# Performance work log

Measured on AMD Instinct MI355X. Metric: run time of the kernel, lower is better.

The kernel has to match this reference:

```python
import jax, jax.numpy as jnp
import numpy as np

E = 1024; H = 16; D = E // H; MAX_LEN = 512; B = 4; N = 1024
EPS = 1e-5
NEG_INF = float('-inf')


def layernorm(x, g, b):
    mu = jnp.mean(x, axis=-1, keepdims=True)
    var = jnp.mean((x - mu) ** 2, axis=-1, keepdims=True)
    return (x - mu) * jax.lax.rsqrt(var + EPS) * g + b


def rel_bias(seq_len, rel_pos):
    # rel_pos: (H, MAX_LEN). bias[h,i,j] = rel_pos[h, i-j] if 0<=i-j<MAX_LEN else -inf
    pos = jnp.arange(seq_len)
    rel = pos[:, None] - pos[None, :]                     # (N, N)
    valid = (rel >= 0) & (rel < rel_pos.shape[-1])
    idx = jnp.clip(rel, 0, rel_pos.shape[-1] - 1)
    gathered = rel_pos[:, idx]                            # (H, N, N)
    return jnp.where(valid[None], gathered, NEG_INF)


def setup_inputs() -> dict:
    key = jax.random.key(0)
    ks = jax.random.split(key, 12)
    s = 0.02
    return {
        'x': jax.random.normal(ks[0], (B, N, E), jnp.float32),
        'rel_pos': jax.random.normal(ks[1], (H, MAX_LEN), jnp.float32),
        'in_proj_w': jax.random.normal(ks[2], (3 * E, E), jnp.float32) * s,
        'in_proj_b': jnp.zeros((3 * E,), jnp.float32),
        'out_w': jax.random.normal(ks[3], (E, E), jnp.float32) * s,
        'out_b': jnp.zeros((E,), jnp.float32),
        'w1': jax.random.normal(ks[4], (4 * E, E), jnp.float32) * s,
        'b1': jnp.zeros((4 * E,), jnp.float32),
        'w2': jax.random.normal(ks[5], (E, 4 * E), jnp.float32) * s,
        'b2': jnp.zeros((E,), jnp.float32),
        'ln1_g': jnp.ones((E,), jnp.float32),
        'ln1_b': jnp.zeros((E,), jnp.float32),
        'ln2_g': jnp.ones((E,), jnp.float32),
        'ln2_b': jnp.zeros((E,), jnp.float32),
    }


def reference(x, rel_pos, in_proj_w, in_proj_b, out_w, out_b,
              w1, b1, w2, b2, ln1_g, ln1_b, ln2_g, ln2_b):
    b, n, e = x.shape
    xn = layernorm(x, ln1_g, ln1_b)
    qkv = xn @ in_proj_w.T + in_proj_b                    # (B, N, 3E)
    q, k, v = jnp.split(qkv, 3, axis=-1)
    # (B, N, E) -> (B, H, N, D)
    def heads(t):
        return t.reshape(b, n, H, D).transpose(0, 2, 1, 3)
    q, k, v = heads(q), heads(k), heads(v)
    bias = rel_bias(n, rel_pos)                           # (H, N, N)
    scores = jnp.einsum('bhnd,bhmd->bhnm', q, k) / np.sqrt(D) + bias[None]
    attn = jax.nn.softmax(scores, axis=-1)
    o = jnp.einsum('bhnm,bhmd->bhnd', attn, v)            # (B, H, N, D)
    o = o.transpose(0, 2, 1, 3).reshape(b, n, e)
    x = x + o @ out_w.T + out_b
    xm = layernorm(x, ln2_g, ln2_b)
    h = jax.nn.relu(xm @ w1.T + b1)
    return x + h @ w2.T + b2
```

## Files before the change

### kernel.cpp

```cpp
#include <hip/hip_runtime.h>
#include <math.h>

#define BB 4
#define NN 1024
#define EE 1024
#define HH 16
#define DD 64
#define MAXLEN 512
#define EPS 1e-5f

typedef __attribute__((ext_vector_type(8))) __bf16 bf16x8;
typedef __attribute__((ext_vector_type(4))) float floatx4;
typedef __attribute__((ext_vector_type(8))) unsigned short ushort8;

#define SWAIT(s) asm volatile("s_waitcnt " s ::: "memory")
#define SCHEDBAR() __builtin_amdgcn_sched_barrier(0)

__device__ __forceinline__ unsigned short f2bf(float f) {
    unsigned u = __float_as_uint(f);
    u += 0x7fffu + ((u >> 16) & 1u);
    return (unsigned short)(u >> 16);
}

template <int MAXR>
__device__ __forceinline__ void vm_wait_rt(int rem) {
    if (rem >= MAXR) {
        if constexpr (MAXR <= 0)      SWAIT("vmcnt(0)");
        else if constexpr (MAXR == 1) SWAIT("vmcnt(4)");
        else if constexpr (MAXR == 2) SWAIT("vmcnt(8)");
        else                          SWAIT("vmcnt(12)");
        return;
    }
    if (rem <= 0) { SWAIT("vmcnt(0)"); return; }
    if (rem == 1) { SWAIT("vmcnt(4)"); return; }
    if constexpr (MAXR >= 3) { if (rem == 2) { SWAIT("vmcnt(8)");  return; } }
}

__global__ __launch_bounds__(256) void f2bf_all_kernel(
    const float* __restrict__ s0, const float* __restrict__ s1,
    const float* __restrict__ s2, const float* __restrict__ s3,
    unsigned short* __restrict__ d0, unsigned short* __restrict__ d1,
    unsigned short* __restrict__ d2, unsigned short* __restrict__ d3) {
    const int C0 = 3 * EE * EE / 4;
    const int C1 = C0 + EE * EE / 4;
    const int C2 = C1 + EE * EE;
    int i = blockIdx.x * 256 + threadIdx.x;
    const float* in; unsigned short* out; int j;
    if (i < C0)      { in = s0; out = d0; j = i; }
    else if (i < C1) { in = s1; out = d1; j = i - C0; }
    else if (i < C2) { in = s2; out = d2; j = i - C1; }
    else             { in = s3; out = d3; j = i - C2; }
    float4 v = ((const float4*)in)[j];
    ushort4 o;
    o.x = f2bf(v.x); o.y = f2bf(v.y); o.z = f2bf(v.z); o.w = f2bf(v.w);
    ((ushort4*)out)[j] = o;
}

__global__ __launch_bounds__(256) void ln_kernel(const float* __restrict__ x,
                                                 const float* __restrict__ g,
                                                 const float* __restrict__ b,
                                                 unsigned short* __restrict__ out) {
    const int row = blockIdx.x;
    const int tid = threadIdx.x;
    const float4 v = ((const float4*)(x + (size_t)row * EE))[tid];
    float s  = v.x + v.y + v.z + v.w;
    float s2 = v.x * v.x + v.y * v.y + v.z * v.z + v.w * v.w;
    for (int off = 32; off > 0; off >>= 1) {
        s  += __shfl_xor(s, off);
        s2 += __shfl_xor(s2, off);
    }
    __shared__ float red[8];
    const int wave = tid >> 6, lane = tid & 63;
    if (lane == 0) { red[wave] = s; red[4 + wave] = s2; }
    __syncthreads();
    s  = red[0] + red[1] + red[2] + red[3];
    s2 = red[4] + red[5] + red[6] + red[7];
    const float mu  = s * (1.0f / EE);
    const float var = s2 * (1.0f / EE) - mu * mu;
    const float inv = rsqrtf(var + EPS);
    const float4 gv = ((const float4*)g)[tid];
    const float4 bv = ((const float4*)b)[tid];
    ushort4 o;
    o.x = f2bf((v.x - mu) * inv * gv.x + bv.x);
    o.y = f2bf((v.y - mu) * inv * gv.y + bv.y);
    o.z = f2bf((v.z - mu) * inv * gv.z + bv.z);
    o.w = f2bf((v.w - mu) * inv * gv.w + bv.w);
    ((ushort4*)(out + (size_t)row * EE))[tid] = o;
}

template <int VARIANT>
__global__ __launch_bounds__(256, 3) void gemm97t_kernel(
    const unsigned short* __restrict__ A,
    const unsigned short* __restrict__ W,
    const float* __restrict__ bias,
    void* __restrict__ Cout, int Nc, int K) {
    __shared__ unsigned short smem[2][8192];

    const int tid  = threadIdx.x;
    const int lane = tid & 63;
    const int wv   = tid >> 6;
    const int wm   = wv >> 1;
    const int wn   = wv & 1;

    int bx = blockIdx.x, by = blockIdx.y;
    {
        const int gx  = gridDim.x;
        const int nwg = gx * gridDim.y;
        const int lin = by * gx + bx;
        const int sl  = (lin & 7) * (nwg >> 3) + (lin >> 3);
        bx = sl % gx; by = sl / gx;
    }
    const int row0 = by * 128;
    const int col0 = bx * 128;
    const int NT   = K >> 5;

    const int srow = lane >> 2;
    const int sq   = ((lane & 3) ^ ((lane >> 3) & 3)) * 8;
    const unsigned short* Ag = A + (size_t)(row0 + srow) * K + sq;
    const unsigned short* Wg = W + (size_t)(col0 + srow) * K + sq;

    auto stage = [&](int t) {
        unsigned short* dst = &smem[t & 1][0];
#pragma unroll
        for (int s = 0; s < 2; ++s) {
            const int r = (wv + s * 4) * 16;
            __builtin_amdgcn_global_load_lds(
                (const __attribute__((address_space(1))) unsigned int*)(Ag + (size_t)r * K + t * 32),
                (__attribute__((address_space(3))) unsigned int*)(dst + r * 32), 16, 0, 0);
        }
#pragma unroll
        for (int s = 0; s < 2; ++s) {
            const int r = (wv + s * 4) * 16;
            __builtin_amdgcn_global_load_lds(
                (const __attribute__((address_space(1))) unsigned int*)(Wg + (size_t)r * K + t * 32),
                (__attribute__((address_space(3))) unsigned int*)(dst + 4096 + r * 32), 16, 0, 0);
        }
    };

    const int frow = lane & 15;
    const int quad = lane >> 4;
    const int rq   = (quad ^ ((frow >> 1) & 3)) * 8;
    const int abase = (wm * 64 + frow) * 32 + rq;
    const int bbase = 4096 + (wn * 64 + frow) * 32 + rq;

    floatx4 acc[4][4];
#pragma unroll
    for (int m = 0; m < 4; ++m)
#pragma unroll
        for (int n = 0; n < 4; ++n) acc[m][n] = (floatx4){0.f, 0.f, 0.f, 0.f};

    stage(0); stage(1);

    for (int t = 0; t < NT; ++t) {
        if (t == NT - 1) { SWAIT("vmcnt(0)"); } else { SWAIT("vmcnt(4)"); }
        __builtin_amdgcn_s_barrier();
        SCHEDBAR();

        const unsigned short* buf = &smem[t & 1][0];
        bf16x8 af0 = *(const bf16x8*)(buf + abase);
        bf16x8 af1 = *(const bf16x8*)(buf + abase + 512);
        bf16x8 af2 = *(const bf16x8*)(buf + abase + 1024);
        bf16x8 af3 = *(const bf16x8*)(buf + abase + 1536);
        bf16x8 bf0 = *(const bf16x8*)(buf + bbase);
        bf16x8 bf1 = *(const bf16x8*)(buf + bbase + 512);
        bf16x8 bf2 = *(const bf16x8*)(buf + bbase + 1024);
        bf16x8 bf3 = *(const bf16x8*)(buf + bbase + 1536);

        __builtin_amdgcn_s_setprio(1);
#pragma unroll
        for (int m = 0; m < 4; ++m)
            acc[m][0] = __builtin_amdgcn_mfma_f32_16x16x32_bf16(
                (m == 0 ? af0 : m == 1 ? af1 : m == 2 ? af2 : af3), bf0, acc[m][0], 0, 0, 0);
#pragma unroll
        for (int m = 0; m < 4; ++m)
            acc[m][1] = __builtin_amdgcn_mfma_f32_16x16x32_bf16(
                (m == 0 ? af0 : m == 1 ? af1 : m == 2 ? af2 : af3), bf1, acc[m][1], 0, 0, 0);
#pragma unroll
        for (int m = 0; m < 4; ++m)
            acc[m][2] = __builtin_amdgcn_mfma_f32_16x16x32_bf16(
                (m == 0 ? af0 : m == 1 ? af1 : m == 2 ? af2 : af3), bf2, acc[m][2], 0, 0, 0);
#pragma unroll
        for (int m = 0; m < 4; ++m)
            acc[m][3] = __builtin_amdgcn_mfma_f32_16x16x32_bf16(
                (m == 0 ? af0 : m == 1 ? af1 : m == 2 ? af2 : af3), bf3, acc[m][3], 0, 0, 0);
        __builtin_amdgcn_s_setprio(0);
        SCHEDBAR();
        __builtin_amdgcn_s_barrier();
        SCHEDBAR();
        if (t + 2 < NT) stage(t + 2);
        SCHEDBAR();
    }

    unsigned short* Cb = (unsigned short*)Cout;
    const int crow = (lane >> 4) * 4;
    const int ccol = lane & 15;
#pragma unroll
    for (int n = 0; n < 4; ++n) {
        const int nn = col0 + wn * 64 + n * 16 + ccol;
        const float bv = bias[nn];
#pragma unroll
        for (int m = 0; m < 4; ++m) {
#pragma unroll
            for (int r = 0; r < 4; ++r) {
                const int mm = row0 + wm * 64 + m * 16 + crow + r;
                float v = acc[m][n][r] + bv;
                if (VARIANT == 1) v = fmaxf(v, 0.f);
                Cb[(size_t)mm * Nc + nn] = f2bf(v);
            }
        }
    }
}

__global__ __launch_bounds__(512, 2) void gemm_kh_kernel(
    const unsigned short* __restrict__ A,
    const unsigned short* __restrict__ W,
    const float* __restrict__ bias,
    const float* res, float* Cout, int Nc, int K) {
    __shared__ unsigned short smem[4][16384];

    const int tid  = threadIdx.x;
    const int lane = tid & 63;
    const int wv   = tid >> 6;
    const int wk   = wv >> 2;
    const int wm   = (wv >> 1) & 1;
    const int wn   = wv & 1;

    int bx = blockIdx.x, by = blockIdx.y;
    {
        const int gx  = gridDim.x;
        const int nwg = gx * gridDim.y;
        const int lin = by * gx + bx;
        const int sl  = (lin & 7) * (nwg >> 3) + (lin >> 3);
        bx = sl % gx; by = sl / gx;
    }
    const int row0 = by * 128;
    const int col0 = bx * 128;
    const int NT   = K >> 6;

    const int srow = lane >> 3;
    const int sq   = ((lane & 7) ^ ((lane >> 3) & 7)) * 8;
    const unsigned short* Ag = A + (size_t)(row0 + srow) * K + sq;
    const unsigned short* Wg = W + (size_t)(col0 + srow) * K + sq;

    auto stage = [&](int t) {
        unsigned short* dst = &smem[t & 3][0];
#pragma unroll
        for (int s = 0; s < 2; ++s) {
            const int r = (wv + s * 8) * 8;
            __builtin_amdgcn_global_load_lds(
                (const __attribute__((address_space(1))) unsigned int*)(Ag + (size_t)r * K + t * 64),
                (__attribute__((address_space(3))) unsigned int*)(dst + r * 64), 16, 0, 0);
        }
#pragma unroll
        for (int s = 0; s < 2; ++s) {
            const int r = (wv + s * 8) * 8;
            __builtin_amdgcn_global_load_lds(
                (const __attribute__((address_space(1))) unsigned int*)(Wg + (size_t)r * K + t * 64),
                (__attribute__((address_space(3))) unsigned int*)(dst + 8192 + r * 64), 16, 0, 0);
        }
    };

    const int frow = lane & 15;
    const int quad = lane >> 4;
    const int phys = ((wk * 4 + quad) ^ (frow & 7)) * 8;
    const int abase = (wm * 64 + frow) * 64 + phys;
    const int bbase = 8192 + (wn * 64 + frow) * 64 + phys;

    floatx4 acc[4][4];
#pragma unroll
    for (int m = 0; m < 4; ++m)
#pragma unroll
        for (int n = 0; n < 4; ++n) acc[m][n] = (floatx4){0.f, 0.f, 0.f, 0.f};

    bf16x8 afA[4], afB[4];

    stage(0); stage(1); stage(2);
    SWAIT("vmcnt(8)");
    __builtin_amdgcn_s_barrier();
    SCHEDBAR();
#pragma unroll
    for (int m = 0; m < 4; ++m)
        afA[m] = *(const bf16x8*)(&smem[0][0] + abase + m * 1024);

#define KH_BODY(T, AFC, AFN, TAIL)                                             \
    {                                                                          \
        const int t_ = (T);                                                    \
        if (!(TAIL)) vm_wait_rt<2>(NT - 2 - t_);                               \
        __builtin_amdgcn_s_barrier();                                          \
        SCHEDBAR();                                                            \
        if (t_ + 3 < NT) stage(t_ + 3);                                        \
        const unsigned short* buf_ = &smem[t_ & 3][0];                         \
        bf16x8 bfr0 = *(const bf16x8*)(buf_ + bbase);                          \
        bf16x8 bfr1 = *(const bf16x8*)(buf_ + bbase + 1024);                   \
        SCHEDBAR();                                                            \
        bf16x8 bfr2 = *(const bf16x8*)(buf_ + bbase + 2048);                   \
        bf16x8 bfr3 = *(const bf16x8*)(buf_ + bbase + 3072);                   \
        if (!(TAIL)) {                                                         \
            const unsigned short* nbuf_ = &smem[(t_ + 1) & 3][0];              \
            _Pragma("unroll")                                                  \
            for (int m = 0; m < 4; ++m)                                        \
                AFN[m] = *(const bf16x8*)(nbuf_ + abase + m * 1024);           \
        }                                                                      \
        SCHEDBAR();                                                            \
        if (TAIL) { SWAIT("lgkmcnt(2)"); } else { SWAIT("lgkmcnt(6)"); }       \
        SCHEDBAR();                                                            \
        __builtin_amdgcn_s_setprio(1);                                         \
        _Pragma("unroll")                                                      \
        for (int m = 0; m < 4; ++m) {                                          \
            acc[m][0] = __builtin_amdgcn_mfma_f32_16x16x32_bf16(               \
                AFC[m], bfr0, acc[m][0], 0, 0, 0);                             \
            acc[m][1] = __builtin_amdgcn_mfma_f32_16x16x32_bf16(               \
                AFC[m], bfr1, acc[m][1], 0, 0, 0);                             \
        }                                                                      \
        SCHEDBAR();                                                            \
        if (TAIL) { SWAIT("lgkmcnt(0)"); } else { SWAIT("lgkmcnt(4)"); }       \
        SCHEDBAR();                                                            \
        _Pragma("unroll")                                                      \
        for (int m = 0; m < 4; ++m) {                                          \
            acc[m][2] = __builtin_amdgcn_mfma_f32_16x16x32_bf16(               \
                AFC[m], bfr2, acc[m][2], 0, 0, 0);                             \
            acc[m][3] = __builtin_amdgcn_mfma_f32_16x16x32_bf16(               \
                AFC[m], bfr3, acc[m][3], 0, 0, 0);                             \
        }                                                                      \
        __builtin_amdgcn_s_setprio(0);                                         \
        SCHEDBAR();                                                            \
    }

    int t = 0;
    for (; t < NT - 2; t += 2) {
        KH_BODY(t,     afA, afB, false);
        KH_BODY(t + 1, afB, afA, false);
    }
    KH_BODY(NT - 2, afA, afB, false);
    KH_BODY(NT - 1, afB, afA, true);
#undef KH_BODY

    __syncthreads();
    float* pbuf = (float*)&smem[0][0];
    const int pair = wm * 2 + wn;
    if (wk == 1) {
#pragma unroll
        for (int m = 0; m < 4; ++m)
#pragma unroll
            for (int n = 0; n < 4; ++n)
                *(floatx4*)&pbuf[pair * 4096 + (m * 4 + n) * 256 + lane * 4] = acc[m][n];
    }
    __syncthreads();
    if (wk == 0) {
        const int crow = (lane >> 4) * 4;
        const int ccol = lane & 15;
#pragma unroll
        for (int n = 0; n < 4; ++n) {
            const int nn = col0 + wn * 64 + n * 16 + ccol;
            const float bv = bias[nn];
#pragma unroll
            for (int m = 0; m < 4; ++m) {
                floatx4 p = *(const floatx4*)&pbuf[pair * 4096 + (m * 4 + n) * 256 + lane * 4];
#pragma unroll
                for (int r = 0; r < 4; ++r) {
                    const int mm = row0 + wm * 64 + m * 16 + crow + r;
                    Cout[(size_t)mm * Nc + nn] =
                        acc[m][n][r] + p[r] + bv + res[(size_t)mm * Nc + nn];
                }
            }
        }
    }
}

__global__ __launch_bounds__(256) void attn_mfma_kernel(
    const unsigned short* __restrict__ qkv,
    const float* __restrict__ rel_pos,
    unsigned short* __restrict__ o) {
    __shared__ unsigned short K_s[2][64][32];
    __shared__ unsigned short V_s[64][72];
    __shared__ unsigned short P_s[4][2][16][32];
    __shared__ float rel_s[MAXLEN];

    const int qt = blockIdx.x, h = blockIdx.y, b = blockIdx.z;
    const int q0 = qt * 64;
    const int tid  = threadIdx.x;
    const int lane = tid & 63;
    const int w    = tid >> 6;
    const int quad = lane >> 4;
    const int c15  = lane & 15;

    rel_s[tid]       = rel_pos[h * MAXLEN + tid];
    rel_s[tid + 256] = rel_pos[h * MAXLEN + tid + 256];

    const size_t rowstride = 3 * EE;
    const size_t base_q = (size_t)(b * NN) * rowstride + h * DD;
    const size_t base_k = base_q + EE;
    const size_t base_v = base_q + 2 * EE;

    bf16x8 aq[2];
    {
        const unsigned short* qrow =
            qkv + base_q + (size_t)(q0 + w * 16 + c15) * rowstride + quad * 8;
        aq[0] = *(const bf16x8*)(qrow);
        aq[1] = *(const bf16x8*)(qrow + 32);
    }

    floatx4 Oacc[4];
#pragma unroll
    for (int j = 0; j < 4; ++j) Oacc[j] = (floatx4){0.f, 0.f, 0.f, 0.f};
    float m_r[4], l_r[4];
#pragma unroll
    for (int r = 0; r < 4; ++r) { m_r[r] = -1e30f; l_r[r] = 0.f; }

    const int jlo = max(0, q0 - (MAXLEN - 1));
    const int c0 = jlo >> 6;
    const int c1 = (q0 + 63) >> 6;

    for (int cc = c0; cc <= c1; ++cc) {
        const int jb0 = cc << 6;
        __syncthreads();

        {
            const int krow = w * 16 + (lane >> 2);
            const int dofs = (lane & 3) * 8;
            const unsigned short* gk =
                qkv + base_k + (size_t)(jb0 + krow) * rowstride + dofs;
            __builtin_amdgcn_global_load_lds(
                (const __attribute__((address_space(1))) unsigned int*)gk,
                (__attribute__((address_space(3))) unsigned int*)&K_s[0][w * 16][0],
                16, 0, 0);
            __builtin_amdgcn_global_load_lds(
                (const __attribute__((address_space(1))) unsigned int*)(gk + 32),
                (__attribute__((address_space(3))) unsigned int*)&K_s[1][w * 16][0],
                16, 0, 0);
        }
        {
            const int key = lane;
            const int d0  = w * 16;
            const unsigned short* gv =
                qkv + base_v + (size_t)(jb0 + key) * rowstride + d0;
            ushort8 va = *(const ushort8*)(gv);
            ushort8 vb = *(const ushort8*)(gv + 8);
#pragma unroll
            for (int ii = 0; ii < 8; ++ii) V_s[d0 + ii][key] = va[ii];
#pragma unroll
            for (int ii = 0; ii < 8; ++ii) V_s[d0 + 8 + ii][key] = vb[ii];
        }
        __syncthreads();

        floatx4 S[4];
#pragma unroll
        for (int jb = 0; jb < 4; ++jb) {
            S[jb] = (floatx4){0.f, 0.f, 0.f, 0.f};
            bf16x8 bk0 = *(const bf16x8*)&K_s[0][jb * 16 + c15][quad * 8];
            bf16x8 bk1 = *(const bf16x8*)&K_s[1][jb * 16 + c15][quad * 8];
            S[jb] = __builtin_amdgcn_mfma_f32_16x16x32_bf16(aq[0], bk0, S[jb], 0, 0, 0);
            S[jb] = __builtin_amdgcn_mfma_f32_16x16x32_bf16(aq[1], bk1, S[jb], 0, 0, 0);
        }

        const int i_base = q0 + w * 16 + quad * 4;
        float sv[4][4];
        float mc[4] = {-1e30f, -1e30f, -1e30f, -1e30f};
#pragma unroll
        for (int jb = 0; jb < 4; ++jb) {
            const int jg = jb0 + jb * 16 + c15;
#pragma unroll
            for (int r = 0; r < 4; ++r) {
                const int rel = (i_base + r) - jg;
                float s;
                if (rel >= 0 && rel < MAXLEN) s = S[jb][r] * 0.125f + rel_s[rel];
                else                          s = -1e30f;
                sv[jb][r] = s;
                mc[r] = fmaxf(mc[r], s);
            }
        }
#pragma unroll
        for (int off = 1; off < 16; off <<= 1)
#pragma unroll
            for (int r = 0; r < 4; ++r) mc[r] = fmaxf(mc[r], __shfl_xor(mc[r], off));

        float alpha[4], psum[4];
#pragma unroll
        for (int r = 0; r < 4; ++r) {
            const float mn = fmaxf(m_r[r], mc[r]);
            alpha[r] = __expf(m_r[r] - mn);
            m_r[r] = mn;
            psum[r] = 0.f;
        }
#pragma unroll
        for (int jb = 0; jb < 4; ++jb)
#pragma unroll
            for (int r = 0; r < 4; ++r) {
                const float p = __expf(sv[jb][r] - m_r[r]);
                sv[jb][r] = p;
                psum[r] += p;
            }
#pragma unroll
        for (int off = 1; off < 16; off <<= 1)
#pragma unroll
            for (int r = 0; r < 4; ++r) psum[r] += __shfl_xor(psum[r], off);
#pragma unroll
        for (int r = 0; r < 4; ++r) l_r[r] = l_r[r] * alpha[r] + psum[r];
#pragma unroll
        for (int jb = 0; jb < 4; ++jb)
#pragma unroll
            for (int r = 0; r < 4; ++r) Oacc[jb][r] *= alpha[r];

#pragma unroll
        for (int jb = 0; jb < 4; ++jb)
#pragma unroll
            for (int r = 0; r < 4; ++r)
                P_s[w][jb >> 1][quad * 4 + r][(jb & 1) * 16 + c15] = f2bf(sv[jb][r]);

        bf16x8 ap0 = *(const bf16x8*)&P_s[w][0][c15][quad * 8];
        bf16x8 ap1 = *(const bf16x8*)&P_s[w][1][c15][quad * 8];

#pragma unroll
        for (int jd = 0; jd < 4; ++jd) {
            bf16x8 bv0 = *(const bf16x8*)&V_s[jd * 16 + c15][quad * 8];
            bf16x8 bv1 = *(const bf16x8*)&V_s[jd * 16 + c15][32 + quad * 8];
            Oacc[jd] = __builtin_amdgcn_mfma_f32_16x16x32_bf16(ap0, bv0, Oacc[jd], 0, 0, 0);
            Oacc[jd] = __builtin_amdgcn_mfma_f32_16x16x32_bf16(ap1, bv1, Oacc[jd], 0, 0, 0);
        }
    }

    float inv[4];
#pragma unroll
    for (int r = 0; r < 4; ++r) inv[r] = 1.0f / l_r[r];
#pragma unroll
    for (int jd = 0; jd < 4; ++jd) {
#pragma unroll
        for (int r = 0; r < 4; ++r) {
            const int row = q0 + w * 16 + quad * 4 + r;
            const int col = h * DD + jd * 16 + c15;
            o[(size_t)(b * NN + row) * EE + col] = f2bf(Oacc[jd][r] * inv[r]);
        }
    }
}

extern "C" void kernel_launch(void* const* d_in, const int* in_sizes, int n_in,
                              void* d_out, int out_size, void* d_ws, size_t ws_size,
                              hipStream_t stream) {
    const float* x         = (const float*)d_in[0];
    const float* rel_pos   = (const float*)d_in[1];
    const float* in_proj_w = (const float*)d_in[2];
    const float* in_proj_b = (const float*)d_in[3];
    const float* out_w     = (const float*)d_in[4];
    const float* out_b     = (const float*)d_in[5];
    const float* w1        = (const float*)d_in[6];
    const float* b1        = (const float*)d_in[7];
    const float* w2        = (const float*)d_in[8];
    const float* b2        = (const float*)d_in[9];
    const float* ln1_g     = (const float*)d_in[10];
    const float* ln1_b     = (const float*)d_in[11];
    const float* ln2_g     = (const float*)d_in[12];
    const float* ln2_b     = (const float*)d_in[13];
    float* out = (float*)d_out;

    char* wsb = (char*)d_ws;
    const size_t MB = 1024 * 1024;
    unsigned short* wqkv_b = (unsigned short*)(wsb + 0);
    unsigned short* wout_b = (unsigned short*)(wsb + 6 * MB);
    unsigned short* w1_b   = (unsigned short*)(wsb + 8 * MB);
    unsigned short* w2_b   = (unsigned short*)(wsb + 16 * MB);
    unsigned short* xn_b   = (unsigned short*)(wsb + 24 * MB);
    unsigned short* qkv_b  = (unsigned short*)(wsb + 32 * MB);
    unsigned short* h_b    = (unsigned short*)(wsb + 32 * MB);
    unsigned short* o_b    = (unsigned short*)(wsb + 56 * MB);

    const int Mrows = BB * NN;

    f2bf_all_kernel<<<3 * EE * EE / 256, 256, 0, stream>>>(
        in_proj_w, out_w, w1, w2, wqkv_b, wout_b, w1_b, w2_b);

    ln_kernel<<<Mrows, 256, 0, stream>>>(x, ln1_g, ln1_b, xn_b);
    gemm97t_kernel<0><<<dim3(3 * EE / 128, Mrows / 128), 256, 0, stream>>>(
        xn_b, wqkv_b, in_proj_b, qkv_b, 3 * EE, EE);
    attn_mfma_kernel<<<dim3(NN / 64, HH, BB), 256, 0, stream>>>(qkv_b, rel_pos, o_b);
    gemm_kh_kernel<<<dim3(EE / 128, Mrows / 128), 512, 0, stream>>>(
        o_b, wout_b, out_b, x, out, EE, EE);
    ln_kernel<<<Mrows, 256, 0, stream>>>(out, ln2_g, ln2_b, xn_b);
    gemm97t_kernel<1><<<dim3(4 * EE / 128, Mrows / 128), 256, 0, stream>>>(
        xn_b, w1_b, b1, h_b, 4 * EE, EE);
    gemm_kh_kernel<<<dim3(EE / 128, Mrows / 128), 512, 0, stream>>>(
        h_b, w2_b, b2, out, out, EE, 4 * EE);
}
```

Baseline: 327.8 us.

## Split-K the FFN down-projection GEMM into two slices with a partial-sum add

The final w2 GEMM (K=4096) now runs as two K-slices over a z-grid dimension, doubling the block count so more CUs are kept busy. The slice that owns the bias and residual writes directly to the output, and the other writes fp32 partials to a workspace region that reuses the space of the already-consumed bf16 weight copies. A separate elementwise kernel then adds the partials into the output. The new GEMM uses a double-buffered shared-memory tile with higher occupancy bounds. In exchange it adds extra fp32 traffic for writing and reading the partials, plus one more kernel launch.

```diff
diff --git a/kernel.cpp b/kernel.cpp
--- a/kernel.cpp
+++ b/kernel.cpp
@@ -56,6 +56,15 @@
     ((ushort4*)out)[j] = o;
 }
 
+__global__ __launch_bounds__(256) void addp_kernel(float* __restrict__ out,
+                                                   const float* __restrict__ p) {
+    const int i = blockIdx.x * 256 + threadIdx.x;
+    float4 a = ((float4*)out)[i];
+    const float4 b = ((const float4*)p)[i];
+    a.x += b.x; a.y += b.y; a.z += b.z; a.w += b.w;
+    ((float4*)out)[i] = a;
+}
+
 __global__ __launch_bounds__(256) void ln_kernel(const float* __restrict__ x,
                                                  const float* __restrict__ g,
                                                  const float* __restrict__ b,
@@ -206,6 +215,150 @@
                 float v = acc[m][n][r] + bv;
                 if (VARIANT == 1) v = fmaxf(v, 0.f);
                 Cb[(size_t)mm * Nc + nn] = f2bf(v);
+            }
+        }
+    }
+}
+
+__global__ __launch_bounds__(512, 4) void gemm_kh2_kernel(
+    const unsigned short* __restrict__ A,
+    const unsigned short* __restrict__ W,
+    const float* __restrict__ bias,
+    const float* __restrict__ res,
+    float* __restrict__ Cout,
+    float* __restrict__ P1,
+    int Nc, int K, int Kslice) {
+    __shared__ unsigned short smem[2][16384];
+
+    const int tid  = threadIdx.x;
+    const int lane = tid & 63;
+    const int wv   = tid >> 6;
+    const int wk   = wv >> 2;
+    const int wm   = (wv >> 1) & 1;
+    const int wn   = wv & 1;
+
+    int bx = blockIdx.x, by = blockIdx.y;
+    {
+        const int gx  = gridDim.x;
+        const int nwg = gx * gridDim.y;
+        const int lin = by * gx + bx;
+        const int sl  = (lin & 7) * (nwg >> 3) + (lin >> 3);
+        bx = sl % gx; by = sl / gx;
+    }
+    const int row0 = by * 128;
+    const int col0 = bx * 128;
+    const int kbase = blockIdx.z * Kslice;
+    const int NT   = Kslice >> 6;
+
+    const int srow = lane >> 3;
+    const int sq   = ((lane & 7) ^ ((lane >> 3) & 7)) * 8;
+    const unsigned short* Ag = A + (size_t)(row0 + srow) * K + kbase + sq;
+    const unsigned short* Wg = W + (size_t)(col0 + srow) * K + kbase + sq;
+
+    auto stage = [&](int t) {
+        unsigned short* dst = &smem[t & 1][0];
+#pragma unroll
+        for (int s = 0; s < 2; ++s) {
+            const int r = (wv + s * 8) * 8;
+            __builtin_amdgcn_global_load_lds(
+                (const __attribute__((address_space(1))) unsigned int*)(Ag + (size_t)r * K + t * 64),
+                (__attribute__((address_space(3))) unsigned int*)(dst + r * 64), 16, 0, 0);
+        }
+#pragma unroll
+        for (int s = 0; s < 2; ++s) {
+            const int r = (wv + s * 8) * 8;
+            __builtin_amdgcn_global_load_lds(
+                (const __attribute__((address_space(1))) unsigned int*)(Wg + (size_t)r * K + t * 64),
+                (__attribute__((address_space(3))) unsigned int*)(dst + 8192 + r * 64), 16, 0, 0);
+        }
+    };
+
+    const int frow = lane & 15;
+    const int quad = lane >> 4;
+    const int phys = ((wk * 4 + quad) ^ (frow & 7)) * 8;
+    const int abase = (wm * 64 + frow) * 64 + phys;
+    const int bbase = 8192 + (wn * 64 + frow) * 64 + phys;
+
+    floatx4 acc[4][4];
+#pragma unroll
+    for (int m = 0; m < 4; ++m)
+#pragma unroll
+        for (int n = 0; n < 4; ++n) acc[m][n] = (floatx4){0.f, 0.f, 0.f, 0.f};
+
+    stage(0); stage(1);
+
+    for (int t = 0; t < NT; ++t) {
+        if (t == NT - 1) { SWAIT("vmcnt(0)"); } else { SWAIT("vmcnt(4)"); }
+        __builtin_amdgcn_s_barrier();
+        SCHEDBAR();
+
+        const unsigned short* buf = &smem[t & 1][0];
+        bf16x8 af0 = *(const bf16x8*)(buf + abase);
+        bf16x8 af1 = *(const bf16x8*)(buf + abase + 1024);
+        bf16x8 af2 = *(const bf16x8*)(buf + abase + 2048);
+        bf16x8 af3 = *(const bf16x8*)(buf + abase + 3072);
+        bf16x8 bf0 = *(const bf16x8*)(buf + bbase);
+        bf16x8 bf1 = *(const bf16x8*)(buf + bbase + 1024);
+        bf16x8 bf2 = *(const bf16x8*)(buf + bbase + 2048);
+        bf16x8 bf3 = *(const bf16x8*)(buf + bbase + 3072);
+
+        __builtin_amdgcn_s_setprio(1);
+#pragma unroll
+        for (int m = 0; m < 4; ++m)
+            acc[m][0] = __builtin_amdgcn_mfma_f32_16x16x32_bf16(
+                (m == 0 ? af0 : m == 1 ? af1 : m == 2 ? af2 : af3), bf0, acc[m][0], 0, 0, 0);
+#pragma unroll
+        for (int m = 0; m < 4; ++m)
+            acc[m][1] = __builtin_amdgcn_mfma_f32_16x16x32_bf16(
+                (m == 0 ? af0 : m == 1 ? af1 : m == 2 ? af2 : af3), bf1, acc[m][1], 0, 0, 0);
+#pragma unroll
+        for (int m = 0; m < 4; ++m)
+            acc[m][2] = __builtin_amdgcn_mfma_f32_16x16x32_bf16(
+                (m == 0 ? af0 : m == 1 ? af1 : m == 2 ? af2 : af3), bf2, acc[m][2], 0, 0, 0);
+#pragma unroll
+        for (int m = 0; m < 4; ++m)
+            acc[m][3] = __builtin_amdgcn_mfma_f32_16x16x32_bf16(
+                (m == 0 ? af0 : m == 1 ? af1 : m == 2 ? af2 : af3), bf3, acc[m][3], 0, 0, 0);
+        __builtin_amdgcn_s_setprio(0);
+        SCHEDBAR();
+        __builtin_amdgcn_s_barrier();
+        SCHEDBAR();
+        if (t + 2 < NT) stage(t + 2);
+        SCHEDBAR();
+    }
+
+    __syncthreads();
+    float* pbuf = (float*)&smem[0][0];
+    const int pair = wm * 2 + wn;
+    if (wk == 1) {
+#pragma unroll
+        for (int m = 0; m < 4; ++m)
+#pragma unroll
+            for (int n = 0; n < 4; ++n)
+                *(floatx4*)&pbuf[pair * 4096 + (m * 4 + n) * 256 + lane * 4] = acc[m][n];
+    }
+    __syncthreads();
+    if (wk == 0) {
+        const int crow = (lane >> 4) * 4;
+        const int ccol = lane & 15;
+        const bool final_z = (blockIdx.z == 0);
+#pragma unroll
+        for (int n = 0; n < 4; ++n) {
+            const int nn = col0 + wn * 64 + n * 16 + ccol;
+            const float bv = final_z ? bias[nn] : 0.f;
+#pragma unroll
+            for (int m = 0; m < 4; ++m) {
+                floatx4 p = *(const floatx4*)&pbuf[pair * 4096 + (m * 4 + n) * 256 + lane * 4];
+#pragma unroll
+                for (int r = 0; r < 4; ++r) {
+                    const int mm = row0 + wm * 64 + m * 16 + crow + r;
+                    const float v = acc[m][n][r] + p[r];
+                    if (final_z) {
+                        Cout[(size_t)mm * Nc + nn] = v + bv + res[(size_t)mm * Nc + nn];
+                    } else {
+                        P1[(size_t)mm * Nc + nn] = v;
+                    }
+                }
             }
         }
     }
@@ -562,6 +715,7 @@
     unsigned short* qkv_b  = (unsigned short*)(wsb + 32 * MB);
     unsigned short* h_b    = (unsigned short*)(wsb + 32 * MB);
     unsigned short* o_b    = (unsigned short*)(wsb + 56 * MB);
+    float* p1 = (float*)(wsb + 0);
 
     const int Mrows = BB * NN;
 
@@ -577,6 +731,7 @@
     ln_kernel<<<Mrows, 256, 0, stream>>>(out, ln2_g, ln2_b, xn_b);
     gemm97t_kernel<1><<<dim3(4 * EE / 128, Mrows / 128), 256, 0, stream>>>(
         xn_b, w1_b, b1, h_b, 4 * EE, EE);
-    gemm_kh_kernel<<<dim3(EE / 128, Mrows / 128), 512, 0, stream>>>(
-        h_b, w2_b, b2, out, out, EE, 4 * EE);
-}
+    gemm_kh2_kernel<<<dim3(EE / 128, Mrows / 128, 2), 512, 0, stream>>>(
+        h_b, w2_b, b2, out, out, p1, EE, 4 * EE, 2 * EE);
+    addp_kernel<<<Mrows * EE / 1024, 256, 0, stream>>>(out, p1);
+}
```

Result: slower. 343.5 us (+4.8%).

## Double-buffer K/V tiles in attention with swizzled K layout and reversed tile order

Applied to the files above, without the earlier changes.

The attention kernel now prefetches the next key chunk's K tile (via global_load_lds) and V registers into a second LDS buffer while computing the current chunk. This removes one barrier per iteration and hides global-load latency behind the MFMA work. K's LDS layout gets an XOR swizzle and P_s gets padding, both to cut LDS bank conflicts. Query tiles are also launched in reverse order so the longer (later) tiles start first, improving load balance. The cost is doubled LDS use for K and V, which may lower occupancy.

```diff
diff --git a/kernel.cpp b/kernel.cpp
--- a/kernel.cpp
+++ b/kernel.cpp
@@ -371,12 +371,13 @@
     const unsigned short* __restrict__ qkv,
     const float* __restrict__ rel_pos,
     unsigned short* __restrict__ o) {
-    __shared__ unsigned short K_s[2][64][32];
-    __shared__ unsigned short V_s[64][72];
-    __shared__ unsigned short P_s[4][2][16][32];
+    __shared__ unsigned short K_s[2][2][64][32];
+    __shared__ unsigned short V_s[2][64][72];
+    __shared__ unsigned short P_s[4][2][16][40];
     __shared__ float rel_s[MAXLEN];
 
-    const int qt = blockIdx.x, h = blockIdx.y, b = blockIdx.z;
+    const int qt = (gridDim.x - 1) - blockIdx.x;
+    const int h = blockIdx.y, b = blockIdx.z;
     const int q0 = qt * 64;
     const int tid  = threadIdx.x;
     const int lane = tid & 63;
@@ -400,6 +401,36 @@
         aq[1] = *(const bf16x8*)(qrow + 32);
     }
 
+    const int krow = w * 16 + (lane >> 2);
+    const int kswz = ((lane & 3) ^ ((lane >> 3) & 3)) * 8;
+    auto stageK = [&](int jb0, int buf) {
+        const unsigned short* gk =
+            qkv + base_k + (size_t)(jb0 + krow) * rowstride + kswz;
+        __builtin_amdgcn_global_load_lds(
+            (const __attribute__((address_space(1))) unsigned int*)gk,
+            (__attribute__((address_space(3))) unsigned int*)&K_s[buf][0][w * 16][0],
+            16, 0, 0);
+        __builtin_amdgcn_global_load_lds(
+            (const __attribute__((address_space(1))) unsigned int*)(gk + 32),
+            (__attribute__((address_space(3))) unsigned int*)&K_s[buf][1][w * 16][0],
+            16, 0, 0);
+    };
+
+    ushort8 va, vb;
+    auto loadV = [&](int jb0) {
+        const unsigned short* gv =
+            qkv + base_v + (size_t)(jb0 + lane) * rowstride + w * 16;
+        va = *(const ushort8*)(gv);
+        vb = *(const ushort8*)(gv + 8);
+    };
+    auto writeV = [&](int buf) {
+        const int d0 = w * 16;
+#pragma unroll
+        for (int ii = 0; ii < 8; ++ii) V_s[buf][d0 + ii][lane] = va[ii];
+#pragma unroll
+        for (int ii = 0; ii < 8; ++ii) V_s[buf][d0 + 8 + ii][lane] = vb[ii];
+    };
+
     floatx4 Oacc[4];
 #pragma unroll
     for (int j = 0; j < 4; ++j) Oacc[j] = (floatx4){0.f, 0.f, 0.f, 0.f};
@@ -411,44 +442,27 @@
     const int c0 = jlo >> 6;
     const int c1 = (q0 + 63) >> 6;
 
+    stageK(c0 << 6, 0);
+    loadV(c0 << 6);
+    writeV(0);
+
     for (int cc = c0; cc <= c1; ++cc) {
         const int jb0 = cc << 6;
+        const int buf = (cc - c0) & 1;
         __syncthreads();
 
-        {
-            const int krow = w * 16 + (lane >> 2);
-            const int dofs = (lane & 3) * 8;
-            const unsigned short* gk =
-                qkv + base_k + (size_t)(jb0 + krow) * rowstride + dofs;
-            __builtin_amdgcn_global_load_lds(
-                (const __attribute__((address_space(1))) unsigned int*)gk,
-                (__attribute__((address_space(3))) unsigned int*)&K_s[0][w * 16][0],
-                16, 0, 0);
-            __builtin_amdgcn_global_load_lds(
-                (const __attribute__((address_space(1))) unsigned int*)(gk + 32),
-                (__attribute__((address_space(3))) unsigned int*)&K_s[1][w * 16][0],
-                16, 0, 0);
-        }
-        {
-            const int key = lane;
-            const int d0  = w * 16;
-            const unsigned short* gv =
-                qkv + base_v + (size_t)(jb0 + key) * rowstride + d0;
-            ushort8 va = *(const ushort8*)(gv);
-            ushort8 vb = *(const ushort8*)(gv + 8);
-#pragma unroll
-            for (int ii = 0; ii < 8; ++ii) V_s[d0 + ii][key] = va[ii];
-#pragma unroll
-            for (int ii = 0; ii < 8; ++ii) V_s[d0 + 8 + ii][key] = vb[ii];
-        }
-        __syncthreads();
+        if (cc < c1) {
+            loadV((cc + 1) << 6);
+            stageK((cc + 1) << 6, buf ^ 1);
+        }
 
         floatx4 S[4];
 #pragma unroll
         for (int jb = 0; jb < 4; ++jb) {
             S[jb] = (floatx4){0.f, 0.f, 0.f, 0.f};
-            bf16x8 bk0 = *(const bf16x8*)&K_s[0][jb * 16 + c15][quad * 8];
-            bf16x8 bk1 = *(const bf16x8*)&K_s[1][jb * 16 + c15][quad * 8];
+            const int rsw = (quad ^ (((jb * 16 + c15) >> 1) & 3)) * 8;
+            bf16x8 bk0 = *(const bf16x8*)&K_s[buf][0][jb * 16 + c15][rsw];
+            bf16x8 bk1 = *(const bf16x8*)&K_s[buf][1][jb * 16 + c15][rsw];
             S[jb] = __builtin_amdgcn_mfma_f32_16x16x32_bf16(aq[0], bk0, S[jb], 0, 0, 0);
             S[jb] = __builtin_amdgcn_mfma_f32_16x16x32_bf16(aq[1], bk1, S[jb], 0, 0, 0);
         }
@@ -512,11 +526,13 @@
 
 #pragma unroll
         for (int jd = 0; jd < 4; ++jd) {
-            bf16x8 bv0 = *(const bf16x8*)&V_s[jd * 16 + c15][quad * 8];
-            bf16x8 bv1 = *(const bf16x8*)&V_s[jd * 16 + c15][32 + quad * 8];
+            bf16x8 bv0 = *(const bf16x8*)&V_s[buf][jd * 16 + c15][quad * 8];
+            bf16x8 bv1 = *(const bf16x8*)&V_s[buf][jd * 16 + c15][32 + quad * 8];
             Oacc[jd] = __builtin_amdgcn_mfma_f32_16x16x32_bf16(ap0, bv0, Oacc[jd], 0, 0, 0);
             Oacc[jd] = __builtin_amdgcn_mfma_f32_16x16x32_bf16(ap1, bv1, Oacc[jd], 0, 0, 0);
         }
+
+        if (cc < c1) writeV(buf ^ 1);
     }
 
     float inv[4];
```

New measurement: 341.6 us. 4.2% more time.

## Double attention query tile per block and prefetch K/V chunks through registers

Applied to the files above, without the earlier changes.

The attention kernel now runs 512 threads (8 waves) per block on 128 query rows, so each loaded K/V chunk is shared by twice as many queries. The next chunk's K/V is loaded into registers during compute and written to LDS at the top of the next iteration, replacing the direct global-to-LDS loads. K is stored with an XOR swizzle and P_s rows are padded to cut LDS bank conflicts, and blocks are launched in reverse order so the heavier tiles start first. The trade-offs are more register pressure, fewer blocks, and a slightly longer key range per block because of the diagonal band.

```diff
diff --git a/kernel.cpp b/kernel.cpp
--- a/kernel.cpp
+++ b/kernel.cpp
@@ -367,25 +367,25 @@
     }
 }
 
-__global__ __launch_bounds__(256) void attn_mfma_kernel(
+__global__ __launch_bounds__(512, 8) void attn_mfma_kernel(
     const unsigned short* __restrict__ qkv,
     const float* __restrict__ rel_pos,
     unsigned short* __restrict__ o) {
     __shared__ unsigned short K_s[2][64][32];
     __shared__ unsigned short V_s[64][72];
-    __shared__ unsigned short P_s[4][2][16][32];
+    __shared__ unsigned short P_s[8][2][16][40];
     __shared__ float rel_s[MAXLEN];
 
-    const int qt = blockIdx.x, h = blockIdx.y, b = blockIdx.z;
-    const int q0 = qt * 64;
+    const int p = (gridDim.x - 1) - blockIdx.x;
+    const int h = blockIdx.y, b = blockIdx.z;
+    const int q0 = p * 128;
     const int tid  = threadIdx.x;
     const int lane = tid & 63;
     const int w    = tid >> 6;
     const int quad = lane >> 4;
     const int c15  = lane & 15;
 
-    rel_s[tid]       = rel_pos[h * MAXLEN + tid];
-    rel_s[tid + 256] = rel_pos[h * MAXLEN + tid + 256];
+    rel_s[tid] = rel_pos[h * MAXLEN + tid];
 
     const size_t rowstride = 3 * EE;
     const size_t base_q = (size_t)(b * NN) * rowstride + h * DD;
@@ -400,6 +400,25 @@
         aq[1] = *(const bf16x8*)(qrow + 32);
     }
 
+    const int khalf = w >> 2;
+    const int kkey  = (w & 3) * 16 + (lane >> 2);
+    const int klq   = lane & 3;
+    const int kphys = klq ^ ((kkey >> 1) & 3);
+    ushort8 kreg, vreg;
+    auto loadK = [&](int jb0) {
+        kreg = *(const ushort8*)(qkv + base_k + (size_t)(jb0 + kkey) * rowstride
+                                 + khalf * 32 + klq * 8);
+    };
+    auto writeK = [&]() { *(ushort8*)&K_s[khalf][kkey][kphys * 8] = kreg; };
+    auto loadV = [&](int jb0) {
+        vreg = *(const ushort8*)(qkv + base_v + (size_t)(jb0 + lane) * rowstride + w * 8);
+    };
+    auto writeV = [&]() {
+        const int d0 = w * 8;
+#pragma unroll
+        for (int ii = 0; ii < 8; ++ii) V_s[d0 + ii][lane] = vreg[ii];
+    };
+
     floatx4 Oacc[4];
 #pragma unroll
     for (int j = 0; j < 4; ++j) Oacc[j] = (floatx4){0.f, 0.f, 0.f, 0.f};
@@ -409,46 +428,30 @@
 
     const int jlo = max(0, q0 - (MAXLEN - 1));
     const int c0 = jlo >> 6;
-    const int c1 = (q0 + 63) >> 6;
+    const int c1 = (q0 + 127) >> 6;
+
+    loadK(c0 << 6);
+    loadV(c0 << 6);
+
+    const int rsw = (quad ^ ((c15 >> 1) & 3)) * 8;
 
     for (int cc = c0; cc <= c1; ++cc) {
         const int jb0 = cc << 6;
         __syncthreads();
-
-        {
-            const int krow = w * 16 + (lane >> 2);
-            const int dofs = (lane & 3) * 8;
-            const unsigned short* gk =
-                qkv + base_k + (size_t)(jb0 + krow) * rowstride + dofs;
-            __builtin_amdgcn_global_load_lds(
-                (const __attribute__((address_space(1))) unsigned int*)gk,
-                (__attribute__((address_space(3))) unsigned int*)&K_s[0][w * 16][0],
-                16, 0, 0);
-            __builtin_amdgcn_global_load_lds(
-                (const __attribute__((address_space(1))) unsigned int*)(gk + 32),
-                (__attribute__((address_space(3))) unsigned int*)&K_s[1][w * 16][0],
-                16, 0, 0);
-        }
-        {
-            const int key = lane;
-            const int d0  = w * 16;
-            const unsigned short* gv =
-                qkv + base_v + (size_t)(jb0 + key) * rowstride + d0;
-            ushort8 va = *(const ushort8*)(gv);
-            ushort8 vb = *(const ushort8*)(gv + 8);
-#pragma unroll
-            for (int ii = 0; ii < 8; ++ii) V_s[d0 + ii][key] = va[ii];
-#pragma unroll
-            for (int ii = 0; ii < 8; ++ii) V_s[d0 + 8 + ii][key] = vb[ii];
-        }
+        writeK();
+        writeV();
         __syncthreads();
+        if (cc < c1) {
+            loadK((cc + 1) << 6);
+            loadV((cc + 1) << 6);
+        }
 
         floatx4 S[4];
 #pragma unroll
         for (int jb = 0; jb < 4; ++jb) {
             S[jb] = (floatx4){0.f, 0.f, 0.f, 0.f};
-            bf16x8 bk0 = *(const bf16x8*)&K_s[0][jb * 16 + c15][quad * 8];
-            bf16x8 bk1 = *(const bf16x8*)&K_s[1][jb * 16 + c15][quad * 8];
+            bf16x8 bk0 = *(const bf16x8*)&K_s[0][jb * 16 + c15][rsw];
+            bf16x8 bk1 = *(const bf16x8*)&K_s[1][jb * 16 + c15][rsw];
             S[jb] = __builtin_amdgcn_mfma_f32_16x16x32_bf16(aq[0], bk0, S[jb], 0, 0, 0);
             S[jb] = __builtin_amdgcn_mfma_f32_16x16x32_bf16(aq[1], bk1, S[jb], 0, 0, 0);
         }
@@ -486,9 +489,9 @@
         for (int jb = 0; jb < 4; ++jb)
 #pragma unroll
             for (int r = 0; r < 4; ++r) {
-                const float p = __expf(sv[jb][r] - m_r[r]);
-                sv[jb][r] = p;
-                psum[r] += p;
+                const float pv = __expf(sv[jb][r] - m_r[r]);
+                sv[jb][r] = pv;
+                psum[r] += pv;
             }
 #pragma unroll
         for (int off = 1; off < 16; off <<= 1)
@@ -571,7 +574,7 @@
     ln_kernel<<<Mrows, 256, 0, stream>>>(x, ln1_g, ln1_b, xn_b);
     gemm97t_kernel<0><<<dim3(3 * EE / 128, Mrows / 128), 256, 0, stream>>>(
         xn_b, wqkv_b, in_proj_b, qkv_b, 3 * EE, EE);
-    attn_mfma_kernel<<<dim3(NN / 64, HH, BB), 256, 0, stream>>>(qkv_b, rel_pos, o_b);
+    attn_mfma_kernel<<<dim3(NN / 128, HH, BB), 512, 0, stream>>>(qkv_b, rel_pos, o_b);
     gemm_kh_kernel<<<dim3(EE / 128, Mrows / 128), 512, 0, stream>>>(
         o_b, wout_b, out_b, x, out, EE, EE);
     ln_kernel<<<Mrows, 256, 0, stream>>>(out, ln2_g, ln2_b, xn_b);
```

After: 369.1 us. 12.6% more time.
